# Kernel optimization log

Measured on AMD Instinct MI355X. Metric: run time of the kernel, lower is better.

## Reference

```python
import jax, jax.numpy as jnp
from jax import lax
import numpy as np

B, S, F = 256, 2048, 64
H1, H2 = 4, 2  # hidden sizes of the two bidirectional LSTM layers


def _lstm_dir(x, Wih, Whh, bih, bhh, reverse):
    """Single-direction LSTM, PyTorch gate order (i, f, g, o).
    x: [B, S, F_in]; Wih: [4H, F_in]; Whh: [4H, H]; biases: [4H].
    Returns hidden states [B, S, H]."""
    Bsz = x.shape[0]
    H = Whh.shape[1]
    xs = jnp.swapaxes(x, 0, 1)  # [S, B, F_in]
    if reverse:
        xs = xs[::-1]
    # Precompute the input projection for all timesteps (one big GEMM).
    px = jnp.einsum('sbf,gf->sbg', xs, Wih) + bih + bhh  # [S, B, 4H]

    def step(carry, p):
        h, c = carry
        gates = p + h @ Whh.T  # [B, 4H]
        i, f, g, o = jnp.split(gates, 4, axis=-1)
        i = jax.nn.sigmoid(i)
        f = jax.nn.sigmoid(f)
        g = jnp.tanh(g)
        o = jax.nn.sigmoid(o)
        c = f * c + i * g
        h = o * jnp.tanh(c)
        return (h, c), h

    h0 = jnp.zeros((Bsz, H), x.dtype)
    (_, _), hs = lax.scan(step, (h0, h0), px)  # hs: [S, B, H]
    if reverse:
        hs = hs[::-1]
    return jnp.swapaxes(hs, 0, 1)  # [B, S, H]


def _bilstm(x, Wih_f, Whh_f, bih_f, bhh_f, Wih_b, Whh_b, bih_b, bhh_b):
    fwd = _lstm_dir(x, Wih_f, Whh_f, bih_f, bhh_f, reverse=False)
    bwd = _lstm_dir(x, Wih_b, Whh_b, bih_b, bhh_b, reverse=True)
    return jnp.concatenate([fwd, bwd], axis=-1)


def _init_lstm_params(key, in_dim, hidden):
    k = 1.0 / np.sqrt(hidden)
    ks = jax.random.split(key, 8)
    u = lambda kk, shape: jax.random.uniform(kk, shape, jnp.float32, -k, k)
    return dict(
        Wih_f=u(ks[0], (4 * hidden, in_dim)), Whh_f=u(ks[1], (4 * hidden, hidden)),
        bih_f=u(ks[2], (4 * hidden,)), bhh_f=u(ks[3], (4 * hidden,)),
        Wih_b=u(ks[4], (4 * hidden, in_dim)), Whh_b=u(ks[5], (4 * hidden, hidden)),
        bih_b=u(ks[6], (4 * hidden,)), bhh_b=u(ks[7], (4 * hidden,)),
    )


def setup_inputs() -> dict:
    key = jax.random.key(0)
    kx, k1, k2 = jax.random.split(key, 3)
    x = jax.random.normal(kx, (B, S, F), dtype=jnp.float32)
    p1 = _init_lstm_params(k1, F, H1)        # layer1: input 64 -> hidden 4, bidir
    p2 = _init_lstm_params(k2, 2 * H1, H2)   # layer2: input 8  -> hidden 2, bidir
    inp = {'x': x}
    for name, v in p1.items():
        inp['l1_' + name] = v
    for name, v in p2.items():
        inp['l2_' + name] = v
    return inp


def reference(x,
              l1_Wih_f, l1_Whh_f, l1_bih_f, l1_bhh_f,
              l1_Wih_b, l1_Whh_b, l1_bih_b, l1_bhh_b,
              l2_Wih_f, l2_Whh_f, l2_bih_f, l2_bhh_f,
              l2_Wih_b, l2_Whh_b, l2_bih_b, l2_bhh_b):
    h = _bilstm(x, l1_Wih_f, l1_Whh_f, l1_bih_f, l1_bhh_f,
                l1_Wih_b, l1_Whh_b, l1_bih_b, l1_bhh_b)   # [B, S, 8]
    out = _bilstm(h, l2_Wih_f, l2_Whh_f, l2_bih_f, l2_bhh_f,
                  l2_Wih_b, l2_Whh_b, l2_bih_b, l2_bhh_b)  # [B, S, 4]
    return out
```

## Files before the change

### kernel.cpp

```cpp
#include <hip/hip_runtime.h>


#define DEVINL __device__ __forceinline__

constexpr int Bn = 256, Sn = 2048;
constexpr int C1 = 64, L1n = Sn / C1, W1n = 40;
constexpr int C2 = 64, L2n = Sn / C2, W2n = 40;

typedef __attribute__((ext_vector_type(8))) short short8;
typedef __attribute__((ext_vector_type(4))) float v4f;

DEVINL float sigm(float x)  { return 1.0f / (1.0f + __expf(-x)); }
DEVINL float tanhx(float x) { return 1.0f - 2.0f / (1.0f + __expf(2.0f * x)); }

template<int CTRL>
DEVINL float qperm(float v) {
    return __int_as_float(
        __builtin_amdgcn_update_dpp(0, __float_as_int(v), CTRL, 0xf, 0xf, true));
}

DEVINL short f2bf(float f) {
    unsigned u = __float_as_uint(f);
    return (short)((u + 0x7fffu + ((u >> 16) & 1u)) >> 16);
}
DEVINL float bf2f(unsigned short u) { return __uint_as_float((unsigned)u << 16); }

DEVINL short8 pack8(float4 a, float4 b) {
    short8 r;
    r[0] = f2bf(a.x); r[1] = f2bf(a.y); r[2] = f2bf(a.z); r[3] = f2bf(a.w);
    r[4] = f2bf(b.x); r[5] = f2bf(b.y); r[6] = f2bf(b.z); r[7] = f2bf(b.w);
    return r;
}

__global__ __launch_bounds__(256) void px1_kernel(
    const float* __restrict__ x,
    const float* __restrict__ WihF, const float* __restrict__ bihF, const float* __restrict__ bhhF,
    const float* __restrict__ WihB, const float* __restrict__ bihB, const float* __restrict__ bhhB,
    unsigned short* __restrict__ px1)
{
    const int lane = threadIdx.x & 63, wv = threadIdx.x >> 6;
    const int n = lane & 15, q = lane >> 4;
    const int r0 = (n & 3) * 4 + ((n >> 2) & 3);

    const float4* WF = reinterpret_cast<const float4*>(WihF + r0 * 64);
    const float4* WB = reinterpret_cast<const float4*>(WihB + r0 * 64);
    const short8 bF0 = pack8(WF[q * 2], WF[q * 2 + 1]);
    const short8 bF1 = pack8(WF[8 + q * 2], WF[8 + q * 2 + 1]);
    const short8 bB0 = pack8(WB[q * 2], WB[q * 2 + 1]);
    const short8 bB1 = pack8(WB[8 + q * 2], WB[8 + q * 2 + 1]);
    const float biasF = bihF[r0] + bhhF[r0], biasB = bihB[r0] + bhhB[r0];

    const size_t row = (size_t)blockIdx.x * 64 + wv * 16 + n;
    const float4* xr = reinterpret_cast<const float4*>(x + row * 64);
    const short8 a0 = pack8(xr[q * 2], xr[q * 2 + 1]);
    const short8 a1 = pack8(xr[8 + q * 2], xr[8 + q * 2 + 1]);

    v4f accF = {biasF, biasF, biasF, biasF};
    v4f accB = {biasB, biasB, biasB, biasB};
    accF = __builtin_amdgcn_mfma_f32_16x16x32_bf16(a0, bF0, accF, 0, 0, 0);
    accF = __builtin_amdgcn_mfma_f32_16x16x32_bf16(a1, bF1, accF, 0, 0, 0);
    accB = __builtin_amdgcn_mfma_f32_16x16x32_bf16(a0, bB0, accB, 0, 0, 0);
    accB = __builtin_amdgcn_mfma_f32_16x16x32_bf16(a1, bB1, accB, 0, 0, 0);

    const size_t rbase = (size_t)blockIdx.x * 64 + wv * 16 + q * 4;
#pragma unroll
    for (int r = 0; r < 4; ++r) {
        px1[(rbase + r) * 32 + n]      = (unsigned short)f2bf(accF[r]);
        px1[(rbase + r) * 32 + 16 + n] = (unsigned short)f2bf(accB[r]);
    }
}

__global__ __launch_bounds__(256) void lstm1_kernel(
    const unsigned short* __restrict__ px1,
    const float* __restrict__ WhhF, const float* __restrict__ WhhB,
    float* __restrict__ h1out)
{
    const int t = blockIdx.x * 256 + threadIdx.x;
    const int j = t & 3;
    const int chain = t >> 2;
    const int chunk = chain & (C1 - 1);
    const int b = (chain >> 6) & (Bn - 1);
    const int d = chain >> 14;
    const float* Whh = d ? WhhB : WhhF;

    float wv[4][4];
#pragma unroll
    for (int ty = 0; ty < 4; ++ty)
#pragma unroll
        for (int c = 0; c < 4; ++c) wv[ty][c] = Whh[(ty * 4 + j) * 4 + c];

    const int sd = d ? -1 : 1;
    const int sb = chunk * L1n;
    const int s_start = d ? (sb + L1n - 1 + W1n) : (sb - W1n);
    const unsigned short* pbase = px1 + (size_t)b * Sn * 32 + (d * 16 + j * 4);

    auto ldp = [&](int ss) -> ushort4 {
        const int sc = ss < 0 ? 0 : (ss > Sn - 1 ? Sn - 1 : ss);
        return *reinterpret_cast<const ushort4*>(pbase + (size_t)sc * 32);
    };

    float h0 = 0.f, h1v = 0.f, h2v = 0.f, h3v = 0.f, cc = 0.f;
    int s = s_start;
    int spf = s_start + 4 * sd;
    ushort4 r0 = ldp(s_start), r1 = ldp(s_start + sd),
            r2 = ldp(s_start + 2 * sd), r3 = ldp(s_start + 3 * sd);

#define STEP1(R)                                                                                       \
    {                                                                                                  \
        const ushort4 pu = R; R = ldp(spf); spf += sd;                                                 \
        if ((unsigned)s < (unsigned)Sn) {                                                              \
            const float pvx = bf2f(pu.x), pvy = bf2f(pu.y), pvz = bf2f(pu.z), pvw = bf2f(pu.w);        \
            float ih = fmaf(wv[0][3], h3v, fmaf(wv[0][2], h2v, fmaf(wv[0][1], h1v, fmaf(wv[0][0], h0, pvx)))); \
            float fh = fmaf(wv[1][3], h3v, fmaf(wv[1][2], h2v, fmaf(wv[1][1], h1v, fmaf(wv[1][0], h0, pvy)))); \
            float gh = fmaf(wv[2][3], h3v, fmaf(wv[2][2], h2v, fmaf(wv[2][1], h1v, fmaf(wv[2][0], h0, pvz)))); \
            float oh = fmaf(wv[3][3], h3v, fmaf(wv[3][2], h2v, fmaf(wv[3][1], h1v, fmaf(wv[3][0], h0, pvw)))); \
            const float ig = sigm(ih), fg = sigm(fh), gg = tanhx(gh), og = sigm(oh);                   \
            cc = fmaf(fg, cc, ig * gg);                                                                \
            const float hj = og * tanhx(cc);                                                           \
            h0 = qperm<0x00>(hj); h1v = qperm<0x55>(hj);                                               \
            h2v = qperm<0xAA>(hj); h3v = qperm<0xFF>(hj);                                              \
            if ((unsigned)(s - sb) < (unsigned)L1n)                                                    \
                h1out[((size_t)b * Sn + s) * 8 + d * 4 + j] = hj;                                      \
        }                                                                                              \
        s += sd;                                                                                       \
    }

    constexpr int NS = W1n + L1n;
    for (int i = 0; i < NS; i += 4) { STEP1(r0) STEP1(r1) STEP1(r2) STEP1(r3) }
#undef STEP1
}

__global__ __launch_bounds__(256) void lstm2_kernel(
    const float* __restrict__ h1in,
    const float* __restrict__ WihF, const float* __restrict__ WhhF,
    const float* __restrict__ bihF, const float* __restrict__ bhhF,
    const float* __restrict__ WihB, const float* __restrict__ WhhB,
    const float* __restrict__ bihB, const float* __restrict__ bhhB,
    float* __restrict__ out)
{
    const int t = blockIdx.x * 256 + threadIdx.x;
    const int j = t & 1;
    const int chain = t >> 1;
    const int chunk = chain & (C2 - 1);
    const int b = (chain >> 6) & (Bn - 1);
    const int d = chain >> 14;
    const float* Wih = d ? WihB : WihF;
    const float* Whh = d ? WhhB : WhhF;
    const float* bih = d ? bihB : bihF;
    const float* bhh = d ? bhhB : bhhF;

    float wx[4][8], wh[4][2], bb[4];
#pragma unroll
    for (int ty = 0; ty < 4; ++ty) {
        const int r = ty * 2 + j;
#pragma unroll
        for (int k = 0; k < 8; ++k) wx[ty][k] = Wih[r * 8 + k];
        wh[ty][0] = Whh[r * 2]; wh[ty][1] = Whh[r * 2 + 1];
        bb[ty] = bih[r] + bhh[r];
    }

    const int sd = d ? -1 : 1;
    const int sb = chunk * L2n;
    const int s_start = d ? (sb + L2n - 1 + W2n) : (sb - W2n);
    const float* hbase = h1in + (size_t)b * Sn * 8;

    auto ldh = [&](int ss, float4& a, float4& b2) {
        const int sc = ss < 0 ? 0 : (ss > Sn - 1 ? Sn - 1 : ss);
        const float4* p = reinterpret_cast<const float4*>(hbase + (size_t)sc * 8);
        a = p[0]; b2 = p[1];
    };

    float hA = 0.f, hB = 0.f, cc = 0.f;
    int s = s_start;
    int spf = s_start + 4 * sd;
    float4 qa0, qb0, qa1, qb1, qa2, qb2, qa3, qb3;
    ldh(s_start,          qa0, qb0);
    ldh(s_start + sd,     qa1, qb1);
    ldh(s_start + 2 * sd, qa2, qb2);
    ldh(s_start + 3 * sd, qa3, qb3);

#define DOT8(W, A, B2, BIAS)                                                                           \
    fmaf(W[0], A.x, fmaf(W[1], A.y, fmaf(W[2], A.z, fmaf(W[3], A.w,                                    \
    fmaf(W[4], B2.x, fmaf(W[5], B2.y, fmaf(W[6], B2.z, fmaf(W[7], B2.w, BIAS))))))))

#define STEP2(RA, RB)                                                                                  \
    {                                                                                                  \
        const float4 ha = RA, hb2 = RB;                                                                \
        ldh(spf, RA, RB); spf += sd;                                                                   \
        if ((unsigned)s < (unsigned)Sn) {                                                              \
            const float xi = DOT8(wx[0], ha, hb2, bb[0]);                                              \
            const float xf = DOT8(wx[1], ha, hb2, bb[1]);                                              \
            const float xg = DOT8(wx[2], ha, hb2, bb[2]);                                              \
            const float xo = DOT8(wx[3], ha, hb2, bb[3]);                                              \
            const float ih = fmaf(wh[0][1], hB, fmaf(wh[0][0], hA, xi));                               \
            const float fh = fmaf(wh[1][1], hB, fmaf(wh[1][0], hA, xf));                               \
            const float gh = fmaf(wh[2][1], hB, fmaf(wh[2][0], hA, xg));                               \
            const float oh = fmaf(wh[3][1], hB, fmaf(wh[3][0], hA, xo));                               \
            const float ig = sigm(ih), fg = sigm(fh), gg = tanhx(gh), og = sigm(oh);                   \
            cc = fmaf(fg, cc, ig * gg);                                                                \
            const float hj = og * tanhx(cc);                                                           \
            const float oth = qperm<0xB1>(hj);                                                         \
            hA = j ? oth : hj;                                                                         \
            hB = j ? hj : oth;                                                                         \
            if ((unsigned)(s - sb) < (unsigned)L2n)                                                    \
                out[((size_t)b * Sn + s) * 4 + d * 2 + j] = hj;                                        \
        }                                                                                              \
        s += sd;                                                                                       \
    }

    constexpr int NS = W2n + L2n;
    for (int i = 0; i < NS; i += 4) { STEP2(qa0, qb0) STEP2(qa1, qb1) STEP2(qa2, qb2) STEP2(qa3, qb3) }
#undef STEP2
#undef DOT8
}

extern "C" void kernel_launch(void* const* d_in, const int* in_sizes, int n_in,
                              void* d_out, int out_size, void* d_ws, size_t ws_size,
                              hipStream_t stream)
{
    const float* x        = (const float*)d_in[0];
    const float* l1_Wih_f = (const float*)d_in[1];
    const float* l1_Whh_f = (const float*)d_in[2];
    const float* l1_bih_f = (const float*)d_in[3];
    const float* l1_bhh_f = (const float*)d_in[4];
    const float* l1_Wih_b = (const float*)d_in[5];
    const float* l1_Whh_b = (const float*)d_in[6];
    const float* l1_bih_b = (const float*)d_in[7];
    const float* l1_bhh_b = (const float*)d_in[8];
    const float* l2_Wih_f = (const float*)d_in[9];
    const float* l2_Whh_f = (const float*)d_in[10];
    const float* l2_bih_f = (const float*)d_in[11];
    const float* l2_bhh_f = (const float*)d_in[12];
    const float* l2_Wih_b = (const float*)d_in[13];
    const float* l2_Whh_b = (const float*)d_in[14];
    const float* l2_bih_b = (const float*)d_in[15];
    const float* l2_bhh_b = (const float*)d_in[16];

    const size_t px1_elems = (size_t)Bn * Sn * 32;
    const size_t h1_elems  = (size_t)Bn * Sn * 8;
    if (ws_size < px1_elems * 2 + h1_elems * 4 + 256) return;

    unsigned short* px1 = (unsigned short*)d_ws;
    float* h1 = (float*)((char*)d_ws + ((px1_elems * 2 + 255) & ~(size_t)255));
    float* out = (float*)d_out;

    px1_kernel<<<dim3(Bn * Sn / 64), 256, 0, stream>>>(
        x, l1_Wih_f, l1_bih_f, l1_bhh_f, l1_Wih_b, l1_bih_b, l1_bhh_b, px1);

    lstm1_kernel<<<dim3(Bn * 2 * C1 * 4 / 256), 256, 0, stream>>>(
        px1, l1_Whh_f, l1_Whh_b, h1);

    lstm2_kernel<<<dim3(Bn * 2 * C2 * 2 / 256), 256, 0, stream>>>(
        h1, l2_Wih_f, l2_Whh_f, l2_bih_f, l2_bhh_f,
        l2_Wih_b, l2_Whh_b, l2_bih_b, l2_bhh_b, out);
}
```

Measured before the change: 284.5 us.

## Double sequence chunks, store h1 in bf16, coalesce px1 writes via LDS

Measured after the change: 301.6 us. 1.06x slower.

```diff
diff --git a/kernel.cpp b/kernel.cpp
--- a/kernel.cpp
+++ b/kernel.cpp
@@ -4,10 +4,11 @@
 #define DEVINL __device__ __forceinline__
 
 constexpr int Bn = 256, Sn = 2048;
-constexpr int C1 = 64, L1n = Sn / C1, W1n = 40;
-constexpr int C2 = 64, L2n = Sn / C2, W2n = 40;
+constexpr int C1 = 128, L1n = Sn / C1, W1n = 40;
+constexpr int C2 = 128, L2n = Sn / C2, W2n = 40;
 
 typedef __attribute__((ext_vector_type(8))) short short8;
+typedef __attribute__((ext_vector_type(8))) unsigned short u16x8;
 typedef __attribute__((ext_vector_type(4))) float v4f;
 
 DEVINL float sigm(float x)  { return 1.0f / (1.0f + __expf(-x)); }
@@ -19,16 +20,16 @@
         __builtin_amdgcn_update_dpp(0, __float_as_int(v), CTRL, 0xf, 0xf, true));
 }
 
-DEVINL short f2bf(float f) {
+DEVINL unsigned short f2bf(float f) {
     unsigned u = __float_as_uint(f);
-    return (short)((u + 0x7fffu + ((u >> 16) & 1u)) >> 16);
+    return (unsigned short)((u + 0x7fffu + ((u >> 16) & 1u)) >> 16);
 }
 DEVINL float bf2f(unsigned short u) { return __uint_as_float((unsigned)u << 16); }
 
 DEVINL short8 pack8(float4 a, float4 b) {
     short8 r;
-    r[0] = f2bf(a.x); r[1] = f2bf(a.y); r[2] = f2bf(a.z); r[3] = f2bf(a.w);
-    r[4] = f2bf(b.x); r[5] = f2bf(b.y); r[6] = f2bf(b.z); r[7] = f2bf(b.w);
+    r[0] = (short)f2bf(a.x); r[1] = (short)f2bf(a.y); r[2] = (short)f2bf(a.z); r[3] = (short)f2bf(a.w);
+    r[4] = (short)f2bf(b.x); r[5] = (short)f2bf(b.y); r[6] = (short)f2bf(b.z); r[7] = (short)f2bf(b.w);
     return r;
 }
 
@@ -38,6 +39,7 @@
     const float* __restrict__ WihB, const float* __restrict__ bihB, const float* __restrict__ bhhB,
     unsigned short* __restrict__ px1)
 {
+    __shared__ unsigned short lds[64 * 32];
     const int lane = threadIdx.x & 63, wv = threadIdx.x >> 6;
     const int n = lane & 15, q = lane >> 4;
     const int r0 = (n & 3) * 4 + ((n >> 2) & 3);
@@ -62,25 +64,30 @@
     accB = __builtin_amdgcn_mfma_f32_16x16x32_bf16(a0, bB0, accB, 0, 0, 0);
     accB = __builtin_amdgcn_mfma_f32_16x16x32_bf16(a1, bB1, accB, 0, 0, 0);
 
-    const size_t rbase = (size_t)blockIdx.x * 64 + wv * 16 + q * 4;
+    const int rowt = wv * 16 + q * 4;
 #pragma unroll
     for (int r = 0; r < 4; ++r) {
-        px1[(rbase + r) * 32 + n]      = (unsigned short)f2bf(accF[r]);
-        px1[(rbase + r) * 32 + 16 + n] = (unsigned short)f2bf(accB[r]);
-    }
+        lds[(rowt + r) * 32 + n]      = f2bf(accF[r]);
+        lds[(rowt + r) * 32 + 16 + n] = f2bf(accB[r]);
+    }
+    __syncthreads();
+
+    const int orow = threadIdx.x >> 2, half = threadIdx.x & 3;
+    const u16x8 v = *reinterpret_cast<const u16x8*>(&lds[orow * 32 + half * 8]);
+    *reinterpret_cast<u16x8*>(px1 + ((size_t)blockIdx.x * 64 + orow) * 32 + half * 8) = v;
 }
 
 __global__ __launch_bounds__(256) void lstm1_kernel(
     const unsigned short* __restrict__ px1,
     const float* __restrict__ WhhF, const float* __restrict__ WhhB,
-    float* __restrict__ h1out)
+    unsigned short* __restrict__ h1out)
 {
     const int t = blockIdx.x * 256 + threadIdx.x;
     const int j = t & 3;
     const int chain = t >> 2;
     const int chunk = chain & (C1 - 1);
-    const int b = (chain >> 6) & (Bn - 1);
-    const int d = chain >> 14;
+    const int b = (chain >> 7) & (Bn - 1);
+    const int d = chain >> 15;
     const float* Whh = d ? WhhB : WhhF;
 
     float wv[4][4];
@@ -101,9 +108,11 @@
 
     float h0 = 0.f, h1v = 0.f, h2v = 0.f, h3v = 0.f, cc = 0.f;
     int s = s_start;
-    int spf = s_start + 4 * sd;
-    ushort4 r0 = ldp(s_start), r1 = ldp(s_start + sd),
-            r2 = ldp(s_start + 2 * sd), r3 = ldp(s_start + 3 * sd);
+    int spf = s_start + 8 * sd;
+    ushort4 r0 = ldp(s_start),          r1 = ldp(s_start + sd),
+            r2 = ldp(s_start + 2 * sd), r3 = ldp(s_start + 3 * sd),
+            r4 = ldp(s_start + 4 * sd), r5 = ldp(s_start + 5 * sd),
+            r6 = ldp(s_start + 6 * sd), r7 = ldp(s_start + 7 * sd);
 
 #define STEP1(R)                                                                                       \
     {                                                                                                  \
@@ -120,18 +129,20 @@
             h0 = qperm<0x00>(hj); h1v = qperm<0x55>(hj);                                               \
             h2v = qperm<0xAA>(hj); h3v = qperm<0xFF>(hj);                                              \
             if ((unsigned)(s - sb) < (unsigned)L1n)                                                    \
-                h1out[((size_t)b * Sn + s) * 8 + d * 4 + j] = hj;                                      \
+                h1out[((size_t)b * Sn + s) * 8 + d * 4 + j] = f2bf(hj);                                \
         }                                                                                              \
         s += sd;                                                                                       \
     }
 
     constexpr int NS = W1n + L1n;
-    for (int i = 0; i < NS; i += 4) { STEP1(r0) STEP1(r1) STEP1(r2) STEP1(r3) }
+    for (int i = 0; i < NS; i += 8) {
+        STEP1(r0) STEP1(r1) STEP1(r2) STEP1(r3) STEP1(r4) STEP1(r5) STEP1(r6) STEP1(r7)
+    }
 #undef STEP1
 }
 
 __global__ __launch_bounds__(256) void lstm2_kernel(
-    const float* __restrict__ h1in,
+    const unsigned short* __restrict__ h1in,
     const float* __restrict__ WihF, const float* __restrict__ WhhF,
     const float* __restrict__ bihF, const float* __restrict__ bhhF,
     const float* __restrict__ WihB, const float* __restrict__ WhhB,
@@ -142,8 +153,8 @@
     const int j = t & 1;
     const int chain = t >> 1;
     const int chunk = chain & (C2 - 1);
-    const int b = (chain >> 6) & (Bn - 1);
-    const int d = chain >> 14;
+    const int b = (chain >> 7) & (Bn - 1);
+    const int d = chain >> 15;
     const float* Wih = d ? WihB : WihF;
     const float* Whh = d ? WhhB : WhhF;
     const float* bih = d ? bihB : bihF;
@@ -162,36 +173,36 @@
     const int sd = d ? -1 : 1;
     const int sb = chunk * L2n;
     const int s_start = d ? (sb + L2n - 1 + W2n) : (sb - W2n);
-    const float* hbase = h1in + (size_t)b * Sn * 8;
-
-    auto ldh = [&](int ss, float4& a, float4& b2) {
+    const unsigned short* hbase = h1in + (size_t)b * Sn * 8;
+
+    auto ldh = [&](int ss) -> u16x8 {
         const int sc = ss < 0 ? 0 : (ss > Sn - 1 ? Sn - 1 : ss);
-        const float4* p = reinterpret_cast<const float4*>(hbase + (size_t)sc * 8);
-        a = p[0]; b2 = p[1];
+        return *reinterpret_cast<const u16x8*>(hbase + (size_t)sc * 8);
     };
 
     float hA = 0.f, hB = 0.f, cc = 0.f;
     int s = s_start;
-    int spf = s_start + 4 * sd;
-    float4 qa0, qb0, qa1, qb1, qa2, qb2, qa3, qb3;
-    ldh(s_start,          qa0, qb0);
-    ldh(s_start + sd,     qa1, qb1);
-    ldh(s_start + 2 * sd, qa2, qb2);
-    ldh(s_start + 3 * sd, qa3, qb3);
-
-#define DOT8(W, A, B2, BIAS)                                                                           \
-    fmaf(W[0], A.x, fmaf(W[1], A.y, fmaf(W[2], A.z, fmaf(W[3], A.w,                                    \
-    fmaf(W[4], B2.x, fmaf(W[5], B2.y, fmaf(W[6], B2.z, fmaf(W[7], B2.w, BIAS))))))))
-
-#define STEP2(RA, RB)                                                                                  \
+    int spf = s_start + 8 * sd;
+    u16x8 q0 = ldh(s_start),          q1 = ldh(s_start + sd),
+          q2 = ldh(s_start + 2 * sd), q3 = ldh(s_start + 3 * sd),
+          q4 = ldh(s_start + 4 * sd), q5 = ldh(s_start + 5 * sd),
+          q6 = ldh(s_start + 6 * sd), q7 = ldh(s_start + 7 * sd);
+
+#define STEP2(R)                                                                                       \
     {                                                                                                  \
-        const float4 ha = RA, hb2 = RB;                                                                \
-        ldh(spf, RA, RB); spf += sd;                                                                   \
+        const u16x8 hu = R; R = ldh(spf); spf += sd;                                                   \
         if ((unsigned)s < (unsigned)Sn) {                                                              \
-            const float xi = DOT8(wx[0], ha, hb2, bb[0]);                                              \
-            const float xf = DOT8(wx[1], ha, hb2, bb[1]);                                              \
-            const float xg = DOT8(wx[2], ha, hb2, bb[2]);                                              \
-            const float xo = DOT8(wx[3], ha, hb2, bb[3]);                                              \
+            float hv[8];                                                                               \
+            _Pragma("unroll")                                                                          \
+            for (int k = 0; k < 8; ++k) hv[k] = bf2f(hu[k]);                                           \
+            float xi = bb[0], xf = bb[1], xg = bb[2], xo = bb[3];                                      \
+            _Pragma("unroll")                                                                          \
+            for (int k = 0; k < 8; ++k) {                                                              \
+                xi = fmaf(wx[0][k], hv[k], xi);                                                        \
+                xf = fmaf(wx[1][k], hv[k], xf);                                                        \
+                xg = fmaf(wx[2][k], hv[k], xg);                                                        \
+                xo = fmaf(wx[3][k], hv[k], xo);                                                        \
+            }                                                                                          \
             const float ih = fmaf(wh[0][1], hB, fmaf(wh[0][0], hA, xi));                               \
             const float fh = fmaf(wh[1][1], hB, fmaf(wh[1][0], hA, xf));                               \
             const float gh = fmaf(wh[2][1], hB, fmaf(wh[2][0], hA, xg));                               \
@@ -209,9 +220,10 @@
     }
 
     constexpr int NS = W2n + L2n;
-    for (int i = 0; i < NS; i += 4) { STEP2(qa0, qb0) STEP2(qa1, qb1) STEP2(qa2, qb2) STEP2(qa3, qb3) }
+    for (int i = 0; i < NS; i += 8) {
+        STEP2(q0) STEP2(q1) STEP2(q2) STEP2(q3) STEP2(q4) STEP2(q5) STEP2(q6) STEP2(q7)
+    }
 #undef STEP2
-#undef DOT8
 }
 
 extern "C" void kernel_launch(void* const* d_in, const int* in_sizes, int n_in,
@@ -238,10 +250,10 @@
 
     const size_t px1_elems = (size_t)Bn * Sn * 32;
     const size_t h1_elems  = (size_t)Bn * Sn * 8;
-    if (ws_size < px1_elems * 2 + h1_elems * 4 + 256) return;
+    if (ws_size < (px1_elems + h1_elems) * 2 + 256) return;
 
     unsigned short* px1 = (unsigned short*)d_ws;
-    float* h1 = (float*)((char*)d_ws + ((px1_elems * 2 + 255) & ~(size_t)255));
+    unsigned short* h1 = (unsigned short*)((char*)d_ws + ((px1_elems * 2 + 255) & ~(size_t)255));
     float* out = (float*)d_out;
 
     px1_kernel<<<dim3(Bn * Sn / 64), 256, 0, stream>>>(
```
